# Kernel tuning notes

Hardware: AMD Instinct MI355X
Metric: run time of the kernel (lower is better)

## Reference

```python
import jax, jax.numpy as jnp
import numpy as np

N_NODES = 50000
N_EDGES = 500000
F_DIM = 128
N_REL = 8
N_LAYERS = 2
NEG_SLOPE = 0.2  # PyG RGATConv default negative_slope


def setup_inputs() -> dict:
    key = jax.random.key(0)
    ks = jax.random.split(key, 6)
    x = jax.random.normal(ks[0], (N_NODES, F_DIM), dtype=jnp.float32)
    edge_index = jax.random.randint(ks[1], (2, N_EDGES), 0, N_NODES)
    edge_type = jax.random.randint(ks[2], (N_EDGES,), 0, N_REL)
    # Per-layer relation weights [L, R, F_in, F_out], attention vectors q,k [L, F_out, 1], bias [L, F_out]
    W = jax.random.normal(ks[3], (N_LAYERS, N_REL, F_DIM, F_DIM), dtype=jnp.float32) * (1.0 / np.sqrt(F_DIM)).astype(np.float32)
    att_q = jax.random.normal(ks[4], (N_LAYERS, F_DIM, 1), dtype=jnp.float32) * 0.1
    att_k = jax.random.normal(ks[5], (N_LAYERS, F_DIM, 1), dtype=jnp.float32) * 0.1
    bias = jnp.zeros((N_LAYERS, F_DIM), dtype=jnp.float32)
    return {"x": x, "W": W, "att_q": att_q, "att_k": att_k, "bias": bias,
            "edge_index": edge_index, "edge_type": edge_type}


def _segment_softmax(logits, seg, num_segments):
    # Numerically stable softmax over edges grouped by destination node.
    m = jax.ops.segment_max(logits, seg, num_segments=num_segments)
    m = jax.lax.stop_gradient(m)
    e = jnp.exp(logits - m[seg])
    denom = jax.ops.segment_sum(e, seg, num_segments=num_segments)
    return e / (denom[seg] + 1e-16)


def _rgat_layer(h, src, dst, edge_type, W, q, k, b):
    # h: [N, F]; W: [R, F, F]. Project once per relation, then gather per edge
    # (avoids materializing [E, F, F] per-edge weight gathers).
    n = h.shape[0]
    xw = jnp.einsum('nf,rfg->rng', h, W)          # [R, N, F]
    out_j = xw[edge_type, src]                    # [E, F] transformed source feats
    out_i = xw[edge_type, dst]                    # [E, F] transformed dest feats
    # additive self-attention: leaky_relu(q(x_i) + k(x_j)), heads=1, dim=1
    logits = jax.nn.leaky_relu((out_i @ q + out_j @ k)[:, 0], NEG_SLOPE)  # [E]
    alpha = _segment_softmax(logits, dst, n)      # across-relation softmax per dst node
    agg = jax.ops.segment_sum(alpha[:, None] * out_j, dst, num_segments=n)  # [N, F]
    return agg + b


def reference(x, W, att_q, att_k, bias, edge_index, edge_type):
    src, dst = edge_index[0], edge_index[1]
    h = x
    for l in range(W.shape[0]):  # small fixed layer count
        h = _rgat_layer(h, src, dst, edge_type, W[l], att_q[l], att_k[l], bias[l])
        h = jax.nn.relu(h)  # dropout is identity in eval mode
    return h
```

## Files before the change

### kernel.cpp

```cpp
#include <hip/hip_runtime.h>
#include <hip/hip_bf16.h>
#include <hip/hip_fp16.h>

#define N_NODES 50000
#define N_EDGES 500000
#define F_DIM   128
#define N_REL   8
#define N_LAYERS 2
#define NEG_SLOPE 0.2f

#define NBLK_N ((N_NODES + 255) / 256)

typedef _Float16 half8 __attribute__((ext_vector_type(8)));
typedef float f32x4  __attribute__((ext_vector_type(4)));


__device__ inline float lrelu(float l) { return (l > 0.f) ? l : NEG_SLOPE * l; }

__global__ __launch_bounds__(256) void prep_h(const float* __restrict__ H,
                                              _Float16* __restrict__ Hf) {
    const size_t i8 = (size_t)blockIdx.x * 256 + threadIdx.x;
    if (i8 >= (size_t)N_NODES * F_DIM / 8) return;
    const float* src = H + i8 * 8;
    float av[8];
    *(float4*)(av)     = *(const float4*)(src);
    *(float4*)(av + 4) = *(const float4*)(src + 4);
    alignas(16) _Float16 hb[8];
#pragma unroll
    for (int j = 0; j < 8; ++j) hb[j] = (_Float16)av[j];
    *(uint4*)(Hf + i8 * 8) = *(const uint4*)hb;
}

__global__ __launch_bounds__(256) void prep_w(const float* __restrict__ W,
                                              _Float16* __restrict__ Wf) {
    __shared__ float tile[64][F_DIM + 1];
    const int mat = blockIdx.x;
    const float* src = W + (size_t)mat * F_DIM * F_DIM;
    const int t = threadIdx.x;
    for (int hf = 0; hf < 2; ++hf) {
#pragma unroll
        for (int i = 0; i < 8; ++i) {
            int idx = t + i * 256;
            int f = idx >> 5, c4 = idx & 31;
            float4 v = *(const float4*)(src + (size_t)(hf * 64 + f) * F_DIM + c4 * 4);
            *(float4*)&tile[f][c4 * 4] = v;
        }
        __syncthreads();
        int g = t >> 1, fs = (t & 1) * 32;
        for (int c = 0; c < 4; ++c) {
            alignas(16) _Float16 th[8];
#pragma unroll
            for (int j = 0; j < 8; ++j) th[j] = (_Float16)tile[fs + c * 8 + j][g];
            size_t o = ((size_t)mat * F_DIM + g) * F_DIM + hf * 64 + fs + c * 8;
            *(uint4*)(Wf + o) = *(const uint4*)th;
        }
        __syncthreads();
    }
}

#define GBM 512
__global__ __launch_bounds__(256, 2) void gemm_xw(const _Float16* __restrict__ Hf,
                                                  const _Float16* __restrict__ Wf,
                                                  const float* __restrict__ qv_g,
                                                  const float* __restrict__ kv_g,
                                                  __half* __restrict__ xw,
                                                  float* __restrict__ a_q,
                                                  float* __restrict__ a_k) {
    __shared__ _Float16 lds[F_DIM * F_DIM];
    const int r   = blockIdx.y;
    const int tid = threadIdx.x;
    const int lane = tid & 63, w = tid >> 6;
    const int q = lane >> 4, ln = lane & 15;

    {
        const _Float16* src = Wf + (size_t)r * F_DIM * F_DIM;
#pragma unroll
        for (int i = 0; i < 8; ++i) {
            int chunk = tid + i * 256;
            int gg = chunk >> 4, c8 = chunk & 15;
            uint4 v = *(const uint4*)(src + gg * F_DIM + c8 * 8);
            *(uint4*)(lds + gg * F_DIM + ((c8 ^ (gg & 15)) * 8)) = v;
        }
    }

    float qvl[8], kvl[8];
#pragma unroll
    for (int t = 0; t < 8; ++t) {
        qvl[t] = qv_g[t * 16 + ln];
        kvl[t] = kv_g[t * 16 + ln];
    }

    __syncthreads();

    for (int t4 = 0; t4 < 4; ++t4) {
        const int rb0 = blockIdx.x * GBM + t4 * 128;
        if (rb0 >= N_NODES) break;

        half8 Af[2][4];
#pragma unroll
        for (int rt = 0; rt < 2; ++rt) {
            int row = rb0 + w * 32 + rt * 16 + ln;
            int ar = (row < N_NODES) ? row : (N_NODES - 1);
            const _Float16* hp = Hf + (size_t)ar * F_DIM;
#pragma unroll
            for (int ks = 0; ks < 4; ++ks)
                Af[rt][ks] = *(const half8*)(hp + ks * 32 + q * 8);
        }

        f32x4 acc[2][8];
#pragma unroll
        for (int rt = 0; rt < 2; ++rt)
#pragma unroll
            for (int t = 0; t < 8; ++t) acc[rt][t] = (f32x4)(0.f);

#pragma unroll
        for (int ks = 0; ks < 4; ++ks) {
            const int jx = (((ks * 4 + q) ^ ln)) << 3;
            half8 Bf[8];
#pragma unroll
            for (int c = 0; c < 8; ++c)
                Bf[c] = *(const half8*)(lds + (c * 16 + ln) * F_DIM + jx);
#pragma unroll
            for (int c = 0; c < 8; ++c)
#pragma unroll
                for (int rt = 0; rt < 2; ++rt)
                    acc[rt][c] = __builtin_amdgcn_mfma_f32_16x16x32_f16(Af[rt][ks], Bf[c], acc[rt][c], 0, 0, 0);
        }

#pragma unroll
        for (int rt = 0; rt < 2; ++rt) {
            float pq[4], pk[4];
#pragma unroll
            for (int reg = 0; reg < 4; ++reg) {
                const int row = rb0 + w * 32 + rt * 16 + q * 4 + reg;
                alignas(16) unsigned short hs[8];
                float sq = 0.f, sk = 0.f;
#pragma unroll
                for (int t = 0; t < 8; ++t) {
                    float v = acc[rt][t][reg];
                    __half hv = __float2half(v);
                    hs[t] = *reinterpret_cast<unsigned short*>(&hv);
                    sq = fmaf(v, qvl[t], sq);
                    sk = fmaf(v, kvl[t], sk);
                }
                if (row < N_NODES)
                    *(uint4*)(xw + ((size_t)r * N_NODES + row) * F_DIM + ln * 8) = *(const uint4*)hs;
                pq[reg] = sq; pk[reg] = sk;
            }
#pragma unroll
            for (int reg = 0; reg < 4; ++reg) {
#pragma unroll
                for (int m = 1; m <= 8; m <<= 1) {
                    pq[reg] += __shfl_xor(pq[reg], m);
                    pk[reg] += __shfl_xor(pk[reg], m);
                }
            }
            if (ln == 0) {
#pragma unroll
                for (int reg = 0; reg < 4; ++reg) {
                    const int row = rb0 + w * 32 + rt * 16 + q * 4 + reg;
                    if (row < N_NODES) {
                        a_q[r * N_NODES + row] = pq[reg];
                        a_k[r * N_NODES + row] = pk[reg];
                    }
                }
            }
        }
    }
}


__global__ __launch_bounds__(256) void count_kernel(const int* __restrict__ dstp,
                                                    int* __restrict__ cnt) {
    int e = blockIdx.x * 256 + threadIdx.x;
    if (e < N_EDGES) atomicAdd(cnt + dstp[e], 1);
}

__global__ __launch_bounds__(256) void block_sum_kernel(const int* __restrict__ cnt,
                                                        int* __restrict__ partial) {
    __shared__ int s[256];
    int idx = blockIdx.x * 256 + threadIdx.x;
    int v = (idx < N_NODES) ? cnt[idx] : 0;
    s[threadIdx.x] = v;
    __syncthreads();
    for (int off = 128; off > 0; off >>= 1) {
        if (threadIdx.x < off) s[threadIdx.x] += s[threadIdx.x + off];
        __syncthreads();
    }
    if (threadIdx.x == 0) partial[blockIdx.x] = s[0];
}

__global__ __launch_bounds__(256) void scan_partials_kernel(int* __restrict__ partial,
                                                            int* __restrict__ row_ptr) {
    __shared__ int s[256];
    int t = threadIdx.x;
    int v = (t < NBLK_N) ? partial[t] : 0;
    s[t] = v;
    __syncthreads();
#pragma unroll
    for (int off = 1; off < 256; off <<= 1) {
        int x = (t >= off) ? s[t - off] : 0;
        __syncthreads();
        s[t] += x;
        __syncthreads();
    }
    if (t < NBLK_N) partial[t] = s[t] - v;
    if (t == 0) row_ptr[N_NODES] = N_EDGES;
}

__global__ __launch_bounds__(256) void scan_block_kernel(const int* __restrict__ cnt,
                                                         const int* __restrict__ partial,
                                                         int* __restrict__ row_ptr) {
    __shared__ int s[256];
    int t = threadIdx.x;
    int idx = blockIdx.x * 256 + t;
    int v = (idx < N_NODES) ? cnt[idx] : 0;
    s[t] = v;
    __syncthreads();
#pragma unroll
    for (int off = 1; off < 256; off <<= 1) {
        int x = (t >= off) ? s[t - off] : 0;
        __syncthreads();
        s[t] += x;
        __syncthreads();
    }
    if (idx < N_NODES) row_ptr[idx] = partial[blockIdx.x] + s[t] - v;
}

__global__ __launch_bounds__(256) void scatter_kernel(const int* __restrict__ srcp,
                                                      const int* __restrict__ dstp,
                                                      const int* __restrict__ etp,
                                                      const int* __restrict__ row_ptr,
                                                      int* __restrict__ cursor,
                                                      unsigned* __restrict__ sorted,
                                                      unsigned short* __restrict__ dst16) {
    int e = blockIdx.x * 256 + threadIdx.x;
    if (e >= N_EDGES) return;
    int d = dstp[e];
    int pos = atomicAdd(cursor + d, 1);
    int j = row_ptr[d] + pos;
    sorted[j] = (unsigned)srcp[e] | ((unsigned)etp[e] << 16);
    dst16[j] = (unsigned short)d;
}

__global__ __launch_bounds__(256) void logits_kernel(const float* __restrict__ a_q,
                                                     const float* __restrict__ a_k,
                                                     const unsigned* __restrict__ sorted,
                                                     const unsigned short* __restrict__ dst16,
                                                     float* __restrict__ lgt) {
    int j = blockIdx.x * 256 + threadIdx.x;
    if (j >= N_EDGES) return;
    unsigned p = sorted[j];
    int s = p & 0xffff, t = p >> 16;
    int d = dst16[j];
    lgt[j] = lrelu(a_q[t * N_NODES + d] + a_k[t * N_NODES + s]);
}

__device__ inline void accum8(float* acc, uint4 v, float a) {
    const __half2* h2 = reinterpret_cast<const __half2*>(&v);
#pragma unroll
    for (int t = 0; t < 4; ++t) {
        float2 f = __half22float2(h2[t]);
        acc[t * 2]     = fmaf(a, f.x, acc[t * 2]);
        acc[t * 2 + 1] = fmaf(a, f.y, acc[t * 2 + 1]);
    }
}
__device__ inline const uint4* xwrow(const __half* xw, unsigned p, int ln) {
    return (const uint4*)(xw + (((size_t)(p >> 16)) * N_NODES + (p & 0xffff)) * F_DIM + ln * 8);
}

__global__ __launch_bounds__(256) void agg_fused(const __half* __restrict__ xw,
                                                 const float* __restrict__ lgt,
                                                 const int* __restrict__ row_ptr,
                                                 const unsigned* __restrict__ sorted,
                                                 const float* __restrict__ bias,
                                                 float* __restrict__ outp,
                                                 _Float16* __restrict__ hfp) {
    const int lane = threadIdx.x & 63;
    const int wave = threadIdx.x >> 6;
    const int ql = lane & 15;
    const int d0 = blockIdx.x * 16 + wave * 4;
    if (d0 >= N_NODES) return;
    const int dmy = d0 + (lane >> 4);
    const int dv = (dmy < N_NODES) ? dmy : (N_NODES - 1);
    const int beg = row_ptr[dv], end = row_ptr[dv + 1];
    const int cnt = (dmy < N_NODES) ? (end - beg) : 0;
    int cmax = cnt;
    cmax = max(cmax, __shfl_xor(cmax, 16));
    cmax = max(cmax, __shfl_xor(cmax, 32));

    if (cmax <= 16) {
        unsigned p = 0;
        float ex = 0.f;
        if (ql < cnt) {
            p = sorted[beg + ql];
            ex = __expf(lgt[beg + ql]);
        }
        float acc[8] = {0, 0, 0, 0, 0, 0, 0, 0};
        for (int i = 0; i < cnt; i += 4) {
            unsigned p0 = __shfl(p, i, 16);
            unsigned p1 = __shfl(p, i + 1, 16);
            unsigned p2 = __shfl(p, i + 2, 16);
            unsigned p3 = __shfl(p, i + 3, 16);
            float a0 = __shfl(ex, i, 16);
            float a1 = __shfl(ex, i + 1, 16);
            float a2 = __shfl(ex, i + 2, 16);
            float a3 = __shfl(ex, i + 3, 16);
            uint4 v0 = *xwrow(xw, p0, ql);
            uint4 v1 = *xwrow(xw, p1, ql);
            uint4 v2 = *xwrow(xw, p2, ql);
            uint4 v3 = *xwrow(xw, p3, ql);
            accum8(acc, v0, a0);
            accum8(acc, v1, a1);
            accum8(acc, v2, a2);
            accum8(acc, v3, a3);
        }
        float dsum = ex;
#pragma unroll
        for (int off = 8; off > 0; off >>= 1) dsum += __shfl_xor(dsum, off, 16);

        if (dmy < N_NODES) {
            const float inv = 1.f / (dsum + 1e-16f);
#pragma unroll
            for (int t = 0; t < 8; ++t) {
                const int col = t * 16 + ql;
                const float v = fmaxf(fmaf(acc[t], inv, bias[col]), 0.f);
                if (outp) outp[(size_t)dmy * F_DIM + col] = v;
                if (hfp)  hfp[(size_t)dmy * F_DIM + col] = (_Float16)v;
            }
        }
    } else {
        const int g = lane >> 4, ln = lane & 15;
        for (int h = 0; h < 4; ++h) {
            const int dd = d0 + h;
            if (dd >= N_NODES) continue;
            const int b = __shfl(beg, h * 16);
            const int c = __shfl(cnt, h * 16);
            if (c <= 64) {
                unsigned p = 0;
                float l = -3.4e38f;
                if (lane < c) {
                    p = sorted[b + lane];
                    l = lgt[b + lane];
                }
                float m = l;
#pragma unroll
                for (int off = 32; off > 0; off >>= 1) m = fmaxf(m, __shfl_xor(m, off));
                const float ex = (lane < c) ? __expf(l - m) : 0.f;
                float acc[8] = {0, 0, 0, 0, 0, 0, 0, 0};
                for (int i = 0; i < c; i += 8) {
                    unsigned p0 = __shfl(p, i + g);
                    unsigned p1 = __shfl(p, i + 4 + g);
                    float a0 = __shfl(ex, i + g);
                    float a1 = __shfl(ex, i + 4 + g);
                    uint4 v0 = *xwrow(xw, p0, ln);
                    uint4 v1 = *xwrow(xw, p1, ln);
                    accum8(acc, v0, a0);
                    accum8(acc, v1, a1);
                }
                float dsum = ex;
#pragma unroll
                for (int off = 32; off > 0; off >>= 1) dsum += __shfl_xor(dsum, off);
#pragma unroll
                for (int t = 0; t < 8; ++t) {
                    acc[t] += __shfl_xor(acc[t], 16);
                    acc[t] += __shfl_xor(acc[t], 32);
                }
                const float inv = 1.f / (dsum + 1e-16f);
#pragma unroll
                for (int j = 0; j < 2; ++j) {
                    const int t = g * 2 + j;
                    const int col = t * 16 + ln;
                    const float v = fmaxf(fmaf(acc[t], inv, bias[col]), 0.f);
                    if (outp) outp[(size_t)dd * F_DIM + col] = v;
                    if (hfp)  hfp[(size_t)dd * F_DIM + col] = (_Float16)v;
                }
            } else {
                const int p0 = lane * 2;
                const int c0 = (p0 & 7) * 16 + (p0 >> 3);
                const int c1 = c0 + 16;
                float2 acc = make_float2(bias[c0], bias[c1]);
                float m = -3.4e38f;
                for (int i = b + lane; i < b + c; i += 64) m = fmaxf(m, lgt[i]);
#pragma unroll
                for (int off = 32; off > 0; off >>= 1) m = fmaxf(m, __shfl_xor(m, off));
                float dsum = 0.f;
                for (int i = b + lane; i < b + c; i += 64) dsum += __expf(lgt[i] - m);
#pragma unroll
                for (int off = 32; off > 0; off >>= 1) dsum += __shfl_xor(dsum, off);
                const float inv = 1.f / (dsum + 1e-16f);
                for (int i = b; i < b + c; ++i) {
                    unsigned pp = sorted[i];
                    float alpha = __expf(lgt[i] - m) * inv;
                    const __half2 h2 = *((const __half2*)xw + (((size_t)(pp >> 16)) * N_NODES + (pp & 0xffff)) * (F_DIM / 2) + lane);
                    float2 v = make_float2(__half2float(h2.x), __half2float(h2.y));
                    acc.x = fmaf(alpha, v.x, acc.x);
                    acc.y = fmaf(alpha, v.y, acc.y);
                }
                const float v0 = fmaxf(acc.x, 0.f), v1 = fmaxf(acc.y, 0.f);
                if (outp) { outp[(size_t)dd * F_DIM + c0] = v0; outp[(size_t)dd * F_DIM + c1] = v1; }
                if (hfp)  { hfp[(size_t)dd * F_DIM + c0] = (_Float16)v0; hfp[(size_t)dd * F_DIM + c1] = (_Float16)v1; }
            }
        }
    }
}


extern "C" void kernel_launch(void* const* d_in, const int* in_sizes, int n_in,
                              void* d_out, int out_size, void* d_ws, size_t ws_size,
                              hipStream_t stream) {
    const float* x     = (const float*)d_in[0];
    const float* W     = (const float*)d_in[1];
    const float* att_q = (const float*)d_in[2];
    const float* att_k = (const float*)d_in[3];
    const float* bias  = (const float*)d_in[4];
    const int* ei      = (const int*)d_in[5];
    const int* etp     = (const int*)d_in[6];
    const int* srcp = ei;
    const int* dstp = ei + N_EDGES;
    float* out = (float*)d_out;
    char* ws   = (char*)d_ws;

    size_t off = 0;
    auto alloc = [&](size_t bytes) {
        void* p = ws + off;
        off = (off + bytes + 511) & ~(size_t)511;
        return p;
    };
    __half* xw       = (__half*)alloc((size_t)N_REL * N_NODES * F_DIM * sizeof(__half));
    float* a_q       = (float*)alloc((size_t)N_REL * N_NODES * sizeof(float));
    float* a_k       = (float*)alloc((size_t)N_REL * N_NODES * sizeof(float));
    int* cnt         = (int*)alloc((size_t)2 * N_NODES * sizeof(int));
    int* cursor      = cnt + N_NODES;
    int* row_ptr     = (int*)alloc(((size_t)N_NODES + 1) * sizeof(int));
    int* partial     = (int*)alloc(256 * sizeof(int));
    unsigned* sorted = (unsigned*)alloc((size_t)N_EDGES * sizeof(unsigned));
    unsigned short* dst16 = (unsigned short*)alloc((size_t)N_EDGES * sizeof(unsigned short));
    float* lgt       = (float*)alloc((size_t)N_EDGES * sizeof(float));
    _Float16* Wf     = (_Float16*)alloc((size_t)N_LAYERS * N_REL * F_DIM * F_DIM * sizeof(_Float16));
    _Float16* Hf     = (_Float16*)alloc((size_t)N_NODES * F_DIM * sizeof(_Float16));

    prep_w<<<N_LAYERS * N_REL, 256, 0, stream>>>(W, Wf);
    hipMemsetAsync(cnt, 0, (size_t)2 * N_NODES * 4, stream);
    count_kernel<<<(N_EDGES + 255) / 256, 256, 0, stream>>>(dstp, cnt);
    block_sum_kernel<<<NBLK_N, 256, 0, stream>>>(cnt, partial);
    scan_partials_kernel<<<1, 256, 0, stream>>>(partial, row_ptr);
    scan_block_kernel<<<NBLK_N, 256, 0, stream>>>(cnt, partial, row_ptr);
    scatter_kernel<<<(N_EDGES + 255) / 256, 256, 0, stream>>>(
        srcp, dstp, etp, row_ptr, cursor, sorted, dst16);

    const int grid_h = (N_NODES * F_DIM / 8 + 255) / 256;
    const int grid_m = (N_NODES + GBM - 1) / GBM;
    const int grid_e = (N_EDGES + 255) / 256;
    prep_h<<<grid_h, 256, 0, stream>>>(x, Hf);
    for (int l = 0; l < N_LAYERS; ++l) {
        gemm_xw<<<dim3(grid_m, N_REL), 256, 0, stream>>>(
            Hf, Wf + (size_t)l * N_REL * F_DIM * F_DIM,
            att_q + l * F_DIM, att_k + l * F_DIM,
            xw, a_q, a_k);
        logits_kernel<<<grid_e, 256, 0, stream>>>(a_q, a_k, sorted, dst16, lgt);
        const bool last = (l == N_LAYERS - 1);
        agg_fused<<<(N_NODES + 15) / 16, 256, 0, stream>>>(
            xw, lgt, row_ptr, sorted, bias + l * F_DIM,
            last ? out : nullptr,
            last ? nullptr : Hf);
    }
}
```

Measured before the change: 294.6 us.

## Replace CSR scan with atomic segment allocation and pack exp-logits with edge ids

Replaces the three-kernel prefix scan with a single kernel in which each destination node claims its start offset via atomicAdd on a global counter, so segments are no longer in node order and degree is read from the count array. The logits kernel now computes exp(leaky_relu) directly and stores it packed with the edge's source/relation word as a uint2. The aggregation then reads one array instead of two and skips the per-segment max subtraction. This saves launches and memory passes but drops the max-subtraction stabilisation, which could overflow if logits were large, and the atomic allocation scatters segment placement.

```diff
diff --git a/kernel.cpp b/kernel.cpp
--- a/kernel.cpp
+++ b/kernel.cpp
@@ -176,61 +176,17 @@
     if (e < N_EDGES) atomicAdd(cnt + dstp[e], 1);
 }
 
-__global__ __launch_bounds__(256) void block_sum_kernel(const int* __restrict__ cnt,
-                                                        int* __restrict__ partial) {
-    __shared__ int s[256];
-    int idx = blockIdx.x * 256 + threadIdx.x;
-    int v = (idx < N_NODES) ? cnt[idx] : 0;
-    s[threadIdx.x] = v;
-    __syncthreads();
-    for (int off = 128; off > 0; off >>= 1) {
-        if (threadIdx.x < off) s[threadIdx.x] += s[threadIdx.x + off];
-        __syncthreads();
-    }
-    if (threadIdx.x == 0) partial[blockIdx.x] = s[0];
-}
-
-__global__ __launch_bounds__(256) void scan_partials_kernel(int* __restrict__ partial,
-                                                            int* __restrict__ row_ptr) {
-    __shared__ int s[256];
-    int t = threadIdx.x;
-    int v = (t < NBLK_N) ? partial[t] : 0;
-    s[t] = v;
-    __syncthreads();
-#pragma unroll
-    for (int off = 1; off < 256; off <<= 1) {
-        int x = (t >= off) ? s[t - off] : 0;
-        __syncthreads();
-        s[t] += x;
-        __syncthreads();
-    }
-    if (t < NBLK_N) partial[t] = s[t] - v;
-    if (t == 0) row_ptr[N_NODES] = N_EDGES;
-}
-
-__global__ __launch_bounds__(256) void scan_block_kernel(const int* __restrict__ cnt,
-                                                         const int* __restrict__ partial,
-                                                         int* __restrict__ row_ptr) {
-    __shared__ int s[256];
-    int t = threadIdx.x;
-    int idx = blockIdx.x * 256 + t;
-    int v = (idx < N_NODES) ? cnt[idx] : 0;
-    s[t] = v;
-    __syncthreads();
-#pragma unroll
-    for (int off = 1; off < 256; off <<= 1) {
-        int x = (t >= off) ? s[t - off] : 0;
-        __syncthreads();
-        s[t] += x;
-        __syncthreads();
-    }
-    if (idx < N_NODES) row_ptr[idx] = partial[blockIdx.x] + s[t] - v;
+__global__ __launch_bounds__(256) void alloc_kernel(const int* __restrict__ cnt,
+                                                    int* __restrict__ gtotal,
+                                                    int* __restrict__ row_start) {
+    int d = blockIdx.x * 256 + threadIdx.x;
+    if (d < N_NODES) row_start[d] = atomicAdd(gtotal, cnt[d]);
 }
 
 __global__ __launch_bounds__(256) void scatter_kernel(const int* __restrict__ srcp,
                                                       const int* __restrict__ dstp,
                                                       const int* __restrict__ etp,
-                                                      const int* __restrict__ row_ptr,
+                                                      const int* __restrict__ row_start,
                                                       int* __restrict__ cursor,
                                                       unsigned* __restrict__ sorted,
                                                       unsigned short* __restrict__ dst16) {
@@ -238,7 +194,7 @@
     if (e >= N_EDGES) return;
     int d = dstp[e];
     int pos = atomicAdd(cursor + d, 1);
-    int j = row_ptr[d] + pos;
+    int j = row_start[d] + pos;
     sorted[j] = (unsigned)srcp[e] | ((unsigned)etp[e] << 16);
     dst16[j] = (unsigned short)d;
 }
@@ -247,13 +203,14 @@
                                                      const float* __restrict__ a_k,
                                                      const unsigned* __restrict__ sorted,
                                                      const unsigned short* __restrict__ dst16,
-                                                     float* __restrict__ lgt) {
+                                                     uint2* __restrict__ elgt) {
     int j = blockIdx.x * 256 + threadIdx.x;
     if (j >= N_EDGES) return;
     unsigned p = sorted[j];
     int s = p & 0xffff, t = p >> 16;
     int d = dst16[j];
-    lgt[j] = lrelu(a_q[t * N_NODES + d] + a_k[t * N_NODES + s]);
+    float ex = __expf(lrelu(a_q[t * N_NODES + d] + a_k[t * N_NODES + s]));
+    elgt[j] = make_uint2(p, __float_as_uint(ex));
 }
 
 __device__ inline void accum8(float* acc, uint4 v, float a) {
@@ -270,9 +227,9 @@
 }
 
 __global__ __launch_bounds__(256) void agg_fused(const __half* __restrict__ xw,
-                                                 const float* __restrict__ lgt,
-                                                 const int* __restrict__ row_ptr,
-                                                 const unsigned* __restrict__ sorted,
+                                                 const uint2* __restrict__ elgt,
+                                                 const int* __restrict__ row_start,
+                                                 const int* __restrict__ degp,
                                                  const float* __restrict__ bias,
                                                  float* __restrict__ outp,
                                                  _Float16* __restrict__ hfp) {
@@ -283,21 +240,22 @@
     if (d0 >= N_NODES) return;
     const int dmy = d0 + (lane >> 4);
     const int dv = (dmy < N_NODES) ? dmy : (N_NODES - 1);
-    const int beg = row_ptr[dv], end = row_ptr[dv + 1];
-    const int cnt = (dmy < N_NODES) ? (end - beg) : 0;
-    int cmax = cnt;
+    const int beg = row_start[dv];
+    const int deg = (dmy < N_NODES) ? degp[dv] : 0;
+    int cmax = deg;
     cmax = max(cmax, __shfl_xor(cmax, 16));
     cmax = max(cmax, __shfl_xor(cmax, 32));
 
     if (cmax <= 16) {
         unsigned p = 0;
         float ex = 0.f;
-        if (ql < cnt) {
-            p = sorted[beg + ql];
-            ex = __expf(lgt[beg + ql]);
+        if (ql < deg) {
+            uint2 e = elgt[beg + ql];
+            p = e.x;
+            ex = __uint_as_float(e.y);
         }
         float acc[8] = {0, 0, 0, 0, 0, 0, 0, 0};
-        for (int i = 0; i < cnt; i += 4) {
+        for (int i = 0; i < deg; i += 4) {
             unsigned p0 = __shfl(p, i, 16);
             unsigned p1 = __shfl(p, i + 1, 16);
             unsigned p2 = __shfl(p, i + 2, 16);
@@ -335,18 +293,15 @@
             const int dd = d0 + h;
             if (dd >= N_NODES) continue;
             const int b = __shfl(beg, h * 16);
-            const int c = __shfl(cnt, h * 16);
+            const int c = __shfl(deg, h * 16);
             if (c <= 64) {
                 unsigned p = 0;
-                float l = -3.4e38f;
+                float ex = 0.f;
                 if (lane < c) {
-                    p = sorted[b + lane];
-                    l = lgt[b + lane];
-                }
-                float m = l;
-#pragma unroll
-                for (int off = 32; off > 0; off >>= 1) m = fmaxf(m, __shfl_xor(m, off));
-                const float ex = (lane < c) ? __expf(l - m) : 0.f;
+                    uint2 e = elgt[b + lane];
+                    p = e.x;
+                    ex = __uint_as_float(e.y);
+                }
                 float acc[8] = {0, 0, 0, 0, 0, 0, 0, 0};
                 for (int i = 0; i < c; i += 8) {
                     unsigned p0 = __shfl(p, i + g);
@@ -380,23 +335,23 @@
                 const int c0 = (p0 & 7) * 16 + (p0 >> 3);
                 const int c1 = c0 + 16;
                 float2 acc = make_float2(bias[c0], bias[c1]);
-                float m = -3.4e38f;
-                for (int i = b + lane; i < b + c; i += 64) m = fmaxf(m, lgt[i]);
-#pragma unroll
-                for (int off = 32; off > 0; off >>= 1) m = fmaxf(m, __shfl_xor(m, off));
                 float dsum = 0.f;
-                for (int i = b + lane; i < b + c; i += 64) dsum += __expf(lgt[i] - m);
+                for (int i = b + lane; i < b + c; i += 64)
+                    dsum += __uint_as_float(elgt[i].y);
 #pragma unroll
                 for (int off = 32; off > 0; off >>= 1) dsum += __shfl_xor(dsum, off);
                 const float inv = 1.f / (dsum + 1e-16f);
+                float sx = 0.f, sy = 0.f;
                 for (int i = b; i < b + c; ++i) {
-                    unsigned pp = sorted[i];
-                    float alpha = __expf(lgt[i] - m) * inv;
-                    const __half2 h2 = *((const __half2*)xw + (((size_t)(pp >> 16)) * N_NODES + (pp & 0xffff)) * (F_DIM / 2) + lane);
+                    uint2 e = elgt[i];
+                    float alpha = __uint_as_float(e.y);
+                    const __half2 h2 = *((const __half2*)xw + (((size_t)(e.x >> 16)) * N_NODES + (e.x & 0xffff)) * (F_DIM / 2) + lane);
                     float2 v = make_float2(__half2float(h2.x), __half2float(h2.y));
-                    acc.x = fmaf(alpha, v.x, acc.x);
-                    acc.y = fmaf(alpha, v.y, acc.y);
-                }
+                    sx = fmaf(alpha, v.x, sx);
+                    sy = fmaf(alpha, v.y, sy);
+                }
+                acc.x += sx * inv;
+                acc.y += sy * inv;
                 const float v0 = fmaxf(acc.x, 0.f), v1 = fmaxf(acc.y, 0.f);
                 if (outp) { outp[(size_t)dd * F_DIM + c0] = v0; outp[(size_t)dd * F_DIM + c1] = v1; }
                 if (hfp)  { hfp[(size_t)dd * F_DIM + c0] = (_Float16)v0; hfp[(size_t)dd * F_DIM + c1] = (_Float16)v1; }
@@ -430,24 +385,22 @@
     __half* xw       = (__half*)alloc((size_t)N_REL * N_NODES * F_DIM * sizeof(__half));
     float* a_q       = (float*)alloc((size_t)N_REL * N_NODES * sizeof(float));
     float* a_k       = (float*)alloc((size_t)N_REL * N_NODES * sizeof(float));
-    int* cnt         = (int*)alloc((size_t)2 * N_NODES * sizeof(int));
+    int* cnt         = (int*)alloc(((size_t)2 * N_NODES + 256) * sizeof(int));
     int* cursor      = cnt + N_NODES;
-    int* row_ptr     = (int*)alloc(((size_t)N_NODES + 1) * sizeof(int));
-    int* partial     = (int*)alloc(256 * sizeof(int));
+    int* gtotal      = cnt + 2 * N_NODES;
+    int* row_start   = (int*)alloc((size_t)N_NODES * sizeof(int));
     unsigned* sorted = (unsigned*)alloc((size_t)N_EDGES * sizeof(unsigned));
     unsigned short* dst16 = (unsigned short*)alloc((size_t)N_EDGES * sizeof(unsigned short));
-    float* lgt       = (float*)alloc((size_t)N_EDGES * sizeof(float));
+    uint2* elgt      = (uint2*)alloc((size_t)N_EDGES * sizeof(uint2));
     _Float16* Wf     = (_Float16*)alloc((size_t)N_LAYERS * N_REL * F_DIM * F_DIM * sizeof(_Float16));
     _Float16* Hf     = (_Float16*)alloc((size_t)N_NODES * F_DIM * sizeof(_Float16));
 
     prep_w<<<N_LAYERS * N_REL, 256, 0, stream>>>(W, Wf);
-    hipMemsetAsync(cnt, 0, (size_t)2 * N_NODES * 4, stream);
+    hipMemsetAsync(cnt, 0, ((size_t)2 * N_NODES + 256) * sizeof(int), stream);
     count_kernel<<<(N_EDGES + 255) / 256, 256, 0, stream>>>(dstp, cnt);
-    block_sum_kernel<<<NBLK_N, 256, 0, stream>>>(cnt, partial);
-    scan_partials_kernel<<<1, 256, 0, stream>>>(partial, row_ptr);
-    scan_block_kernel<<<NBLK_N, 256, 0, stream>>>(cnt, partial, row_ptr);
+    alloc_kernel<<<NBLK_N, 256, 0, stream>>>(cnt, gtotal, row_start);
     scatter_kernel<<<(N_EDGES + 255) / 256, 256, 0, stream>>>(
-        srcp, dstp, etp, row_ptr, cursor, sorted, dst16);
+        srcp, dstp, etp, row_start, cursor, sorted, dst16);
 
     const int grid_h = (N_NODES * F_DIM / 8 + 255) / 256;
     const int grid_m = (N_NODES + GBM - 1) / GBM;
@@ -458,10 +411,10 @@
             Hf, Wf + (size_t)l * N_REL * F_DIM * F_DIM,
             att_q + l * F_DIM, att_k + l * F_DIM,
             xw, a_q, a_k);
-        logits_kernel<<<grid_e, 256, 0, stream>>>(a_q, a_k, sorted, dst16, lgt);
+        logits_kernel<<<grid_e, 256, 0, stream>>>(a_q, a_k, sorted, dst16, elgt);
         const bool last = (l == N_LAYERS - 1);
         agg_fused<<<(N_NODES + 15) / 16, 256, 0, stream>>>(
-            xw, lgt, row_ptr, sorted, bias + l * F_DIM,
+            xw, elgt, row_start, cnt, bias + l * F_DIM,
             last ? out : nullptr,
             last ? nullptr : Hf);
     }
```

Result: no change. 297.2 us (+0.9%).
